# Kernel tuning notes

Measured on AMD Instinct MI355X. Metric: run time of the kernel, lower is better.

Reference implementation:

```python
import math
import jax, jax.numpy as jnp
import numpy as np

B, H, L, Dh = 4, 8, 4096, 64
TOPK_FACTOR = 1.0


def setup_inputs() -> dict:
    key = jax.random.key(0)
    kq, kk, kv = jax.random.split(key, 3)
    shape = (B, H, L, Dh)
    return {
        "q": jax.random.normal(kq, shape, dtype=jnp.float32),
        "k": jax.random.normal(kk, shape, dtype=jnp.float32),
        "v": jax.random.normal(kv, shape, dtype=jnp.float32),
    }


def reference(q, k, v):
    b, h, length, dh = q.shape
    # FFT cross-correlation over the time axis, averaged over Dh -> (B,H,L)
    qf = jnp.fft.rfft(q, axis=2)
    kf = jnp.fft.rfft(k, axis=2)
    corr = jnp.fft.irfft(qf * jnp.conj(kf), n=length, axis=2).mean(axis=-1)
    # top-k delays (k_top is static: depends only on L)
    k_top = max(1, int(TOPK_FACTOR * math.log(length + 1)))
    weights, delays = jax.lax.top_k(corr, k_top)  # (B,H,K)
    attn = jax.nn.softmax(weights, axis=-1)       # (B,H,K)
    # circular-shift gather: idx[b,h,t,j] = (t - delay[b,h,j]) mod L
    t = jnp.arange(length)
    idx = (t[None, None, :, None] - delays[:, :, None, :]) % length  # (B,H,L,K)
    # gathered: (B,H,L,K,Dh)
    gathered = jnp.take_along_axis(v[:, :, :, None, :], idx[..., None], axis=2)
    out = (gathered * attn[:, :, None, :, None]).sum(axis=3)  # (B,H,L,Dh)
    return out
```

## Files before the change

kernel.cpp:

```cpp
#include <hip/hip_runtime.h>
#include <math.h>

#define LEN 4096
#define LOG2LEN 12
#define DH 64
#define NBH 32
#define KTOP 8
#define DPB 4
#define NGRP (DH / DPB)

#define ZT_ELEMS ((size_t)NBH * DH * LEN)
#define TW_N (LEN / 2)
#define SPEC_F2 (NBH * LEN)
#define PART_F2 ((size_t)NBH * NGRP * LEN)

#define XSTR 272

__device__ __forceinline__ int rev16_12(int x) {
  return ((x & 15) << 8) | (x & 240) | (x >> 8);
}

template <int SIM>
__device__ __forceinline__ void twget(const float2* __restrict__ tw, int e,
                                      float& wr, float& wi) {
  const float2 t = tw[e & (TW_N - 1)];
  const float sgn = (e & TW_N) ? -1.0f : 1.0f;
  wr = sgn * t.x;
  wi = sgn * (float)SIM * t.y;
}

struct cf { float r, i; };
__device__ __forceinline__ cf cadd(const cf a, const cf b) { return {a.r + b.r, a.i + b.i}; }
__device__ __forceinline__ cf csub(const cf a, const cf b) { return {a.r - b.r, a.i - b.i}; }
__device__ __forceinline__ cf cmul(const cf a, const float wr, const float wi) {
  return {a.r * wr - a.i * wi, a.r * wi + a.i * wr};
}
template <int S>
__device__ __forceinline__ cf cmuli(const cf a) {
  return (S < 0) ? cf{a.i, -a.r} : cf{-a.i, a.r};
}
template <int S>
__device__ __forceinline__ cf twc(const cf a, const float c, const float s) {
  return cmul(a, c, (S < 0) ? -s : s);
}
template <int S>
__device__ __forceinline__ void r4(cf& a, cf& b, cf& c, cf& d) {
  const cf t0 = cadd(a, c), t1 = csub(a, c), t2 = cadd(b, d), t3 = csub(b, d);
  const cf j3 = cmuli<S>(t3);
  a = cadd(t0, t2); c = csub(t0, t2);
  b = cadd(t1, j3); d = csub(t1, j3);
}
template <int S>
__device__ __forceinline__ void dft16(cf* x) {
  r4<S>(x[0], x[4], x[8], x[12]);
  r4<S>(x[1], x[5], x[9], x[13]);
  r4<S>(x[2], x[6], x[10], x[14]);
  r4<S>(x[3], x[7], x[11], x[15]);
  const float C1 = 0.92387953251128675613f;
  const float S1 = 0.38268343236508977173f;
  const float R2 = 0.70710678118654752440f;
  x[5] = twc<S>(x[5], C1, S1);
  x[6] = twc<S>(x[6], R2, R2);
  x[7] = twc<S>(x[7], S1, C1);
  x[9] = twc<S>(x[9], R2, R2);
  x[10] = cmuli<S>(x[10]);
  x[11] = twc<S>(x[11], -R2, R2);
  x[13] = twc<S>(x[13], S1, C1);
  x[14] = twc<S>(x[14], -R2, R2);
  x[15] = twc<S>(x[15], -C1, -S1);
  r4<S>(x[0], x[1], x[2], x[3]);
  r4<S>(x[4], x[5], x[6], x[7]);
  r4<S>(x[8], x[9], x[10], x[11]);
  r4<S>(x[12], x[13], x[14], x[15]);
  cf t;
  t = x[1]; x[1] = x[4]; x[4] = t;
  t = x[2]; x[2] = x[8]; x[8] = t;
  t = x[3]; x[3] = x[12]; x[12] = t;
  t = x[6]; x[6] = x[9]; x[9] = t;
  t = x[7]; x[7] = x[13]; x[13] = t;
  t = x[11]; x[11] = x[14]; x[14] = t;
}

__global__ void ac_twinit(float2* __restrict__ tw) {
  const int j = blockIdx.x * 256 + threadIdx.x;
  if (j < TW_N) {
    float s, c;
    sincosf(6.2831853071795864769f * (float)j / (float)LEN, &s, &c);
    tw[j] = make_float2(c, s);
  }
}

__global__ __launch_bounds__(256, 4) void ac_transpose(const float* __restrict__ q,
                                                       const float* __restrict__ k,
                                                       float2* __restrict__ zT,
                                                       float2* __restrict__ tw) {
  if (blockIdx.x < 8) {
    const int j = blockIdx.x * 256 + threadIdx.x;
    float s, c;
    sincosf(6.2831853071795864769f * (float)j / (float)LEN, &s, &c);
    tw[j] = make_float2(c, s);
  }
  __shared__ float tq[64][65], tk[64][65];
  const int bh = blockIdx.x >> 6;
  const int t0 = (blockIdx.x & 63) * 64;
  const int tid = threadIdx.x;
  const int tl = tid >> 2;
  const int c = tid & 3;
  const float* qb = q + ((size_t)bh * LEN + t0) * DH;
  const float* kb = k + ((size_t)bh * LEN + t0) * DH;
#pragma unroll
  for (int r = 0; r < 4; ++r) {
    const int d0 = (c + r * 4) * 4;
    const float4 vq = *reinterpret_cast<const float4*>(qb + (size_t)tl * DH + d0);
    const float4 vk = *reinterpret_cast<const float4*>(kb + (size_t)tl * DH + d0);
    tq[tl][d0] = vq.x; tq[tl][d0 + 1] = vq.y; tq[tl][d0 + 2] = vq.z; tq[tl][d0 + 3] = vq.w;
    tk[tl][d0] = vk.x; tk[tl][d0 + 1] = vk.y; tk[tl][d0 + 2] = vk.z; tk[tl][d0 + 3] = vk.w;
  }
  __syncthreads();
  const int d = tid >> 2;
  const int s = tid & 3;
  float2* ob = zT + ((size_t)(bh * DH + d)) * LEN + t0;
#pragma unroll
  for (int r = 0; r < 8; ++r) {
    const int t = (s + r * 4) * 2;
    const float4 o = make_float4(tq[t][d], tk[t][d], tq[t + 1][d], tk[t + 1][d]);
    *reinterpret_cast<float4*>(&ob[t]) = o;
  }
}

template <bool TR>
__global__ __launch_bounds__(256, 2) void ac_fft_fwd(const float* __restrict__ q,
                                                     const float* __restrict__ k,
                                                     const float2* __restrict__ zin,
                                                     const float2* __restrict__ tw,
                                                     float2* __restrict__ part) {
  __shared__ float lre[16 * XSTR], lim[16 * XSTR];
  __shared__ float2 acc[LEN];
  const int tid = threadIdx.x;
  const int hi = tid >> 4, lo = tid & 15;
  const int bh = blockIdx.x / NGRP;
  const int g = blockIdx.x % NGRP;

#pragma unroll
  for (int i = 0; i < 16; ++i) acc[tid + 256 * i] = make_float2(0.f, 0.f);

  for (int dd = 0; dd < DPB; ++dd) {
    const int d = g * DPB + dd;
    cf x[16];
    if (TR) {
      const float2* zb = zin + (size_t)(bh * DH + d) * LEN;
#pragma unroll
      for (int n1 = 0; n1 < 16; ++n1) {
        const float2 z = zb[tid + 256 * n1];
        x[n1].r = z.x; x[n1].i = z.y;
      }
    } else {
      const float* qb = q + (size_t)bh * LEN * DH + d;
      const float* kb = k + (size_t)bh * LEN * DH + d;
#pragma unroll
      for (int n1 = 0; n1 < 16; ++n1) {
        x[n1].r = qb[(size_t)(tid + 256 * n1) * DH];
        x[n1].i = kb[(size_t)(tid + 256 * n1) * DH];
      }
    }
    dft16<-1>(x);
#pragma unroll
    for (int k1 = 1; k1 < 16; ++k1) {
      float wr, wi;
      twget<-1>(tw, tid * k1, wr, wi);
      x[k1] = cmul(x[k1], wr, wi);
    }
    __syncthreads();
#pragma unroll
    for (int k1 = 0; k1 < 16; ++k1) {
      lre[k1 * XSTR + tid] = x[k1].r;
      lim[k1 * XSTR + tid] = x[k1].i;
    }
    __syncthreads();
#pragma unroll
    for (int m1 = 0; m1 < 16; ++m1) {
      const int a = hi * XSTR + 16 * m1 + lo;
      x[m1].r = lre[a]; x[m1].i = lim[a];
    }
    dft16<-1>(x);
#pragma unroll
    for (int j1 = 1; j1 < 16; ++j1) {
      float wr, wi;
      twget<-1>(tw, 16 * lo * j1, wr, wi);
      x[j1] = cmul(x[j1], wr, wi);
    }
    __syncthreads();
#pragma unroll
    for (int j1 = 0; j1 < 16; ++j1) {
      lre[hi * XSTR + 16 * j1 + lo] = x[j1].r;
      lim[hi * XSTR + 16 * j1 + lo] = x[j1].i;
    }
    __syncthreads();
#pragma unroll
    for (int m2 = 0; m2 < 16; ++m2) {
      const int a = hi * XSTR + 16 * lo + m2;
      x[m2].r = lre[a]; x[m2].i = lim[a];
    }
    dft16<-1>(x);
    __syncthreads();
#pragma unroll
    for (int j2 = 0; j2 < 16; ++j2) {
      lre[hi * XSTR + 16 * lo + j2] = x[j2].r;
      lim[hi * XSTR + 16 * lo + j2] = x[j2].i;
    }
    __syncthreads();
#pragma unroll
    for (int i = 0; i < 16; ++i) {
      const int p = tid + 256 * i;
      const int f = rev16_12(p);
      const int f2 = (LEN - f) & (LEN - 1);
      const int p2 = rev16_12(f2);
      const int a1 = i * XSTR + tid;
      const int a2 = (p2 >> 8) * XSTR + (p2 & 255);
      const float ar = lre[a1], ai = lim[a1];
      const float br = lre[a2], bi = lim[a2];
      float2 a = acc[p];
      a.x += 0.5f * (ar * bi + ai * br);
      a.y += 0.25f * ((ar * ar + ai * ai) - (br * br + bi * bi));
      acc[p] = a;
    }
  }
  float2* op = part + (size_t)(bh * NGRP + g) * LEN;
#pragma unroll
  for (int i = 0; i < 16; ++i) {
    const int p = tid + 256 * i;
    op[p] = acc[p];
  }
}

__global__ __launch_bounds__(256) void ac_reduce(const float2* __restrict__ part,
                                                 float2* __restrict__ spec) {
  const int bh = blockIdx.x >> 4;
  const int p = ((blockIdx.x & 15) << 8) | threadIdx.x;
  float accr = 0.f, acci = 0.f;
#pragma unroll 4
  for (int g = 0; g < NGRP; ++g) {
    const float2 v = part[((size_t)(bh * NGRP + g) << LOG2LEN) + p];
    accr += v.x; acci += v.y;
  }
  spec[((size_t)bh << LOG2LEN) + p] = make_float2(accr, acci);
}

__global__ __launch_bounds__(256, 4) void ac_fft_inv(const float2* __restrict__ spec,
                                                     const float2* __restrict__ tw,
                                                     float* __restrict__ attn,
                                                     int* __restrict__ delays) {
  __shared__ float lre[16 * XSTR], lim[16 * XSTR];
  __shared__ float rv[256];
  __shared__ int ri[256];
  __shared__ float selv[KTOP];
  __shared__ int seli[KTOP];
  const int bh = blockIdx.x;
  const int tid = threadIdx.x;
  const int hi = tid >> 4, lo = tid & 15;
  const float2* sp = spec + ((size_t)bh << LOG2LEN);

  cf x[16];
#pragma unroll
  for (int f2 = 0; f2 < 16; ++f2) {
    const float2 z = sp[16 * tid + f2];
    x[f2].r = z.x; x[f2].i = z.y;
  }
  dft16<1>(x);
#pragma unroll
  for (int t0 = 1; t0 < 16; ++t0) {
    float wr, wi;
    twget<1>(tw, 16 * lo * t0, wr, wi);
    x[t0] = cmul(x[t0], wr, wi);
  }
#pragma unroll
  for (int t0 = 0; t0 < 16; ++t0) {
    lre[hi * XSTR + 16 * t0 + lo] = x[t0].r;
    lim[hi * XSTR + 16 * t0 + lo] = x[t0].i;
  }
  __syncthreads();
#pragma unroll
  for (int f1 = 0; f1 < 16; ++f1) {
    const int a = hi * XSTR + 16 * lo + f1;
    x[f1].r = lre[a]; x[f1].i = lim[a];
  }
  dft16<1>(x);
#pragma unroll
  for (int t1 = 0; t1 < 16; ++t1) {
    float wr, wi;
    twget<1>(tw, hi * (16 * t1 + lo), wr, wi);
    x[t1] = cmul(x[t1], wr, wi);
  }
  __syncthreads();
#pragma unroll
  for (int t1 = 0; t1 < 16; ++t1) {
    lre[hi * XSTR + 16 * t1 + lo] = x[t1].r;
    lim[hi * XSTR + 16 * t1 + lo] = x[t1].i;
  }
  __syncthreads();
#pragma unroll
  for (int f0 = 0; f0 < 16; ++f0) {
    const int a = f0 * XSTR + 16 * hi + lo;
    x[f0].r = lre[a]; x[f0].i = lim[a];
  }
  dft16<1>(x);
  __syncthreads();
  const float scale = 1.0f / ((float)LEN * (float)DH);
#pragma unroll
  for (int t2 = 0; t2 < 16; ++t2) lre[256 * t2 + tid] = x[t2].r * scale;
  __syncthreads();

  for (int kk = 0; kk < KTOP; ++kk) {
    float mv = -3.0e38f;
    int mi = 0;
    for (int t = tid; t < LEN; t += 256) {
      const float xv = lre[t];
      if (xv > mv) { mv = xv; mi = t; }
    }
    rv[tid] = mv; ri[tid] = mi;
    __syncthreads();
    for (int s = 128; s > 0; s >>= 1) {
      if (tid < s) {
        if (rv[tid + s] > rv[tid]) { rv[tid] = rv[tid + s]; ri[tid] = ri[tid + s]; }
      }
      __syncthreads();
    }
    if (tid == 0) {
      selv[kk] = rv[0];
      seli[kk] = ri[0];
      lre[ri[0]] = -3.0e38f;
    }
    __syncthreads();
  }
  if (tid == 0) {
    const float mx = selv[0];
    float ex[KTOP];
    float sum = 0.f;
    for (int j = 0; j < KTOP; ++j) { ex[j] = expf(selv[j] - mx); sum += ex[j]; }
    const float inv = 1.0f / sum;
    for (int j = 0; j < KTOP; ++j) {
      attn[bh * KTOP + j] = ex[j] * inv;
      delays[bh * KTOP + j] = seli[j];
    }
  }
}

__global__ __launch_bounds__(256) void ac_gather(const float* __restrict__ v,
                                                 const float* __restrict__ attn,
                                                 const int* __restrict__ delays,
                                                 float* __restrict__ out) {
  const int bx = blockIdx.x;
  const int xcd = bx & 7;
  const int i = bx >> 3;
  const int bh = (xcd << 2) | (i & 3);
  const int chunk = i >> 2;
  const int tid = threadIdx.x;
  float aw[KTOP];
  int dl[KTOP];
#pragma unroll
  for (int j = 0; j < KTOP; ++j) {
    aw[j] = attn[bh * KTOP + j];
    dl[j] = delays[bh * KTOP + j];
  }
  const int e = chunk * 1024 + tid * 4;
  const int t = e >> 6;
  const int d = e & 63;
  const float* vb = v + (size_t)bh * LEN * DH;
  float4 acc = make_float4(0.f, 0.f, 0.f, 0.f);
#pragma unroll
  for (int j = 0; j < KTOP; ++j) {
    int src = t - dl[j];
    if (src < 0) src += LEN;
    const float4 vv = *reinterpret_cast<const float4*>(vb + (size_t)src * DH + d);
    acc.x += aw[j] * vv.x;
    acc.y += aw[j] * vv.y;
    acc.z += aw[j] * vv.z;
    acc.w += aw[j] * vv.w;
  }
  *reinterpret_cast<float4*>(out + (size_t)bh * LEN * DH + e) = acc;
}

extern "C" void kernel_launch(void* const* d_in, const int* in_sizes, int n_in,
                              void* d_out, int out_size, void* d_ws, size_t ws_size,
                              hipStream_t stream) {
  const float* q = (const float*)d_in[0];
  const float* k = (const float*)d_in[1];
  const float* v = (const float*)d_in[2];
  float* out = (float*)d_out;

  const size_t need = (size_t)TW_N * 8 + ZT_ELEMS * 8 + PART_F2 * 8 +
                      (size_t)SPEC_F2 * 8 + (size_t)NBH * KTOP * 8;
  const bool tr = (ws_size >= need);

  float2* tw = (float2*)d_ws;
  float2* zT = tw + TW_N;
  float2* part = tr ? (zT + ZT_ELEMS) : zT;
  float2* spec = part + PART_F2;
  float* attn = (float*)(spec + SPEC_F2);
  int* delays = (int*)(attn + NBH * KTOP);

  if (tr) {
    ac_transpose<<<dim3(NBH * 64), dim3(256), 0, stream>>>(q, k, zT, tw);
    ac_fft_fwd<true><<<dim3(NBH * NGRP), dim3(256), 0, stream>>>(q, k, zT, tw, part);
  } else {
    ac_twinit<<<dim3(8), dim3(256), 0, stream>>>(tw);
    ac_fft_fwd<false><<<dim3(NBH * NGRP), dim3(256), 0, stream>>>(q, k, zT, tw, part);
  }
  ac_reduce<<<dim3(NBH * 16), dim3(256), 0, stream>>>(part, spec);
  ac_fft_inv<<<dim3(NBH), dim3(256), 0, stream>>>(spec, tw, attn, delays);
  ac_gather<<<dim3(NBH * 256), dim3(256), 0, stream>>>(v, attn, delays, out);
}
```

Before: 97.50 us.

## Drop transpose, twiddle table and reduce kernels; compute twiddles by recurrence

Removes the transpose kernel and the twiddle-table setup, so the forward FFT reads q/k directly with strided loads. Twiddles are now computed in registers from one sincos per stage plus complex-multiply recurrence instead of being read from a global table. The separate reduce kernel is folded into the inverse FFT, which sums the 16 partial spectra while loading them. Block ids in the forward FFT are remapped to spread tasks differently across the device. This cuts two launches and the intermediate global traffic, at the cost of uncoalesced strided loads, recurrence rounding error in the twiddles, and a serial 16-way reduction inside only 32 blocks.

```diff
diff --git a/kernel.cpp b/kernel.cpp
--- a/kernel.cpp
+++ b/kernel.cpp
@@ -9,24 +9,13 @@
 #define DPB 4
 #define NGRP (DH / DPB)
 
-#define ZT_ELEMS ((size_t)NBH * DH * LEN)
-#define TW_N (LEN / 2)
-#define SPEC_F2 (NBH * LEN)
 #define PART_F2 ((size_t)NBH * NGRP * LEN)
+#define TWO_PI 6.2831853071795864769f
 
 #define XSTR 272
 
 __device__ __forceinline__ int rev16_12(int x) {
   return ((x & 15) << 8) | (x & 240) | (x >> 8);
-}
-
-template <int SIM>
-__device__ __forceinline__ void twget(const float2* __restrict__ tw, int e,
-                                      float& wr, float& wi) {
-  const float2 t = tw[e & (TW_N - 1)];
-  const float sgn = (e & TW_N) ? -1.0f : 1.0f;
-  wr = sgn * t.x;
-  wi = sgn * (float)SIM * t.y;
 }
 
 struct cf { float r, i; };
@@ -81,94 +70,47 @@
   t = x[11]; x[11] = x[14]; x[14] = t;
 }
 
-__global__ void ac_twinit(float2* __restrict__ tw) {
-  const int j = blockIdx.x * 256 + threadIdx.x;
-  if (j < TW_N) {
-    float s, c;
-    sincosf(6.2831853071795864769f * (float)j / (float)LEN, &s, &c);
-    tw[j] = make_float2(c, s);
-  }
-}
-
-__global__ __launch_bounds__(256, 4) void ac_transpose(const float* __restrict__ q,
-                                                       const float* __restrict__ k,
-                                                       float2* __restrict__ zT,
-                                                       float2* __restrict__ tw) {
-  if (blockIdx.x < 8) {
-    const int j = blockIdx.x * 256 + threadIdx.x;
-    float s, c;
-    sincosf(6.2831853071795864769f * (float)j / (float)LEN, &s, &c);
-    tw[j] = make_float2(c, s);
-  }
-  __shared__ float tq[64][65], tk[64][65];
-  const int bh = blockIdx.x >> 6;
-  const int t0 = (blockIdx.x & 63) * 64;
-  const int tid = threadIdx.x;
-  const int tl = tid >> 2;
-  const int c = tid & 3;
-  const float* qb = q + ((size_t)bh * LEN + t0) * DH;
-  const float* kb = k + ((size_t)bh * LEN + t0) * DH;
-#pragma unroll
-  for (int r = 0; r < 4; ++r) {
-    const int d0 = (c + r * 4) * 4;
-    const float4 vq = *reinterpret_cast<const float4*>(qb + (size_t)tl * DH + d0);
-    const float4 vk = *reinterpret_cast<const float4*>(kb + (size_t)tl * DH + d0);
-    tq[tl][d0] = vq.x; tq[tl][d0 + 1] = vq.y; tq[tl][d0 + 2] = vq.z; tq[tl][d0 + 3] = vq.w;
-    tk[tl][d0] = vk.x; tk[tl][d0 + 1] = vk.y; tk[tl][d0 + 2] = vk.z; tk[tl][d0 + 3] = vk.w;
-  }
-  __syncthreads();
-  const int d = tid >> 2;
-  const int s = tid & 3;
-  float2* ob = zT + ((size_t)(bh * DH + d)) * LEN + t0;
-#pragma unroll
-  for (int r = 0; r < 8; ++r) {
-    const int t = (s + r * 4) * 2;
-    const float4 o = make_float4(tq[t][d], tk[t][d], tq[t + 1][d], tk[t + 1][d]);
-    *reinterpret_cast<float4*>(&ob[t]) = o;
-  }
-}
-
-template <bool TR>
 __global__ __launch_bounds__(256, 2) void ac_fft_fwd(const float* __restrict__ q,
                                                      const float* __restrict__ k,
-                                                     const float2* __restrict__ zin,
-                                                     const float2* __restrict__ tw,
                                                      float2* __restrict__ part) {
   __shared__ float lre[16 * XSTR], lim[16 * XSTR];
   __shared__ float2 acc[LEN];
   const int tid = threadIdx.x;
   const int hi = tid >> 4, lo = tid & 15;
-  const int bh = blockIdx.x / NGRP;
-  const int g = blockIdx.x % NGRP;
+  const int bid = (int)blockIdx.x;
+  const int task = ((bid & 7) << 6) | (bid >> 3);
+  const int bh = task >> 4;
+  const int g = task & 15;
+
+  float s1, c1, s2, c2;
+  sincosf(-TWO_PI * (float)tid / (float)LEN, &s1, &c1);
+  sincosf(-TWO_PI * (float)lo / 256.0f, &s2, &c2);
 
 #pragma unroll
   for (int i = 0; i < 16; ++i) acc[tid + 256 * i] = make_float2(0.f, 0.f);
 
+  const float* qb = q + (size_t)bh * LEN * DH + 4 * g;
+  const float* kb = k + (size_t)bh * LEN * DH + 4 * g;
+
+#pragma unroll 1
   for (int dd = 0; dd < DPB; ++dd) {
-    const int d = g * DPB + dd;
     cf x[16];
-    if (TR) {
-      const float2* zb = zin + (size_t)(bh * DH + d) * LEN;
-#pragma unroll
-      for (int n1 = 0; n1 < 16; ++n1) {
-        const float2 z = zb[tid + 256 * n1];
-        x[n1].r = z.x; x[n1].i = z.y;
+#pragma unroll
+    for (int n1 = 0; n1 < 16; ++n1) {
+      const size_t off = (size_t)(tid + 256 * n1) * DH + dd;
+      x[n1].r = qb[off];
+      x[n1].i = kb[off];
+    }
+    dft16<-1>(x);
+    {
+      float cr = c1, ci = s1;
+#pragma unroll
+      for (int k1 = 1; k1 < 16; ++k1) {
+        x[k1] = cmul(x[k1], cr, ci);
+        const float nr = cr * c1 - ci * s1;
+        ci = cr * s1 + ci * c1;
+        cr = nr;
       }
-    } else {
-      const float* qb = q + (size_t)bh * LEN * DH + d;
-      const float* kb = k + (size_t)bh * LEN * DH + d;
-#pragma unroll
-      for (int n1 = 0; n1 < 16; ++n1) {
-        x[n1].r = qb[(size_t)(tid + 256 * n1) * DH];
-        x[n1].i = kb[(size_t)(tid + 256 * n1) * DH];
-      }
-    }
-    dft16<-1>(x);
-#pragma unroll
-    for (int k1 = 1; k1 < 16; ++k1) {
-      float wr, wi;
-      twget<-1>(tw, tid * k1, wr, wi);
-      x[k1] = cmul(x[k1], wr, wi);
     }
     __syncthreads();
 #pragma unroll
@@ -183,11 +125,15 @@
       x[m1].r = lre[a]; x[m1].i = lim[a];
     }
     dft16<-1>(x);
-#pragma unroll
-    for (int j1 = 1; j1 < 16; ++j1) {
-      float wr, wi;
-      twget<-1>(tw, 16 * lo * j1, wr, wi);
-      x[j1] = cmul(x[j1], wr, wi);
+    {
+      float cr = c2, ci = s2;
+#pragma unroll
+      for (int j1 = 1; j1 < 16; ++j1) {
+        x[j1] = cmul(x[j1], cr, ci);
+        const float nr = cr * c2 - ci * s2;
+        ci = cr * s2 + ci * c2;
+        cr = nr;
+      }
     }
     __syncthreads();
 #pragma unroll
@@ -233,21 +179,7 @@
   }
 }
 
-__global__ __launch_bounds__(256) void ac_reduce(const float2* __restrict__ part,
-                                                 float2* __restrict__ spec) {
-  const int bh = blockIdx.x >> 4;
-  const int p = ((blockIdx.x & 15) << 8) | threadIdx.x;
-  float accr = 0.f, acci = 0.f;
-#pragma unroll 4
-  for (int g = 0; g < NGRP; ++g) {
-    const float2 v = part[((size_t)(bh * NGRP + g) << LOG2LEN) + p];
-    accr += v.x; acci += v.y;
-  }
-  spec[((size_t)bh << LOG2LEN) + p] = make_float2(accr, acci);
-}
-
-__global__ __launch_bounds__(256, 4) void ac_fft_inv(const float2* __restrict__ spec,
-                                                     const float2* __restrict__ tw,
+__global__ __launch_bounds__(256, 2) void ac_fft_inv(const float2* __restrict__ part,
                                                      float* __restrict__ attn,
                                                      int* __restrict__ delays) {
   __shared__ float lre[16 * XSTR], lim[16 * XSTR];
@@ -258,20 +190,36 @@
   const int bh = blockIdx.x;
   const int tid = threadIdx.x;
   const int hi = tid >> 4, lo = tid & 15;
-  const float2* sp = spec + ((size_t)bh << LOG2LEN);
 
   cf x[16];
 #pragma unroll
-  for (int f2 = 0; f2 < 16; ++f2) {
-    const float2 z = sp[16 * tid + f2];
-    x[f2].r = z.x; x[f2].i = z.y;
-  }
+  for (int f2 = 0; f2 < 16; ++f2) { x[f2].r = 0.f; x[f2].i = 0.f; }
+  const float2* pb = part + ((size_t)bh * NGRP) * LEN + 16 * tid;
+  for (int g = 0; g < NGRP; ++g) {
+    const float4* b4 = reinterpret_cast<const float4*>(pb + (size_t)g * LEN);
+#pragma unroll
+    for (int i = 0; i < 8; ++i) {
+      const float4 vv = b4[i];
+      x[2 * i].r += vv.x; x[2 * i].i += vv.y;
+      x[2 * i + 1].r += vv.z; x[2 * i + 1].i += vv.w;
+    }
+  }
+
+  float sA, cA, sB0, cB0, sBs, cBs;
+  sincosf(TWO_PI * (float)lo / 256.0f, &sA, &cA);
+  sincosf(TWO_PI * (float)(hi * lo) / (float)LEN, &sB0, &cB0);
+  sincosf(TWO_PI * (float)hi / 256.0f, &sBs, &cBs);
+
   dft16<1>(x);
-#pragma unroll
-  for (int t0 = 1; t0 < 16; ++t0) {
-    float wr, wi;
-    twget<1>(tw, 16 * lo * t0, wr, wi);
-    x[t0] = cmul(x[t0], wr, wi);
+  {
+    float cr = cA, ci = sA;
+#pragma unroll
+    for (int t0 = 1; t0 < 16; ++t0) {
+      x[t0] = cmul(x[t0], cr, ci);
+      const float nr = cr * cA - ci * sA;
+      ci = cr * sA + ci * cA;
+      cr = nr;
+    }
   }
 #pragma unroll
   for (int t0 = 0; t0 < 16; ++t0) {
@@ -285,11 +233,15 @@
     x[f1].r = lre[a]; x[f1].i = lim[a];
   }
   dft16<1>(x);
-#pragma unroll
-  for (int t1 = 0; t1 < 16; ++t1) {
-    float wr, wi;
-    twget<1>(tw, hi * (16 * t1 + lo), wr, wi);
-    x[t1] = cmul(x[t1], wr, wi);
+  {
+    float cr = cB0, ci = sB0;
+#pragma unroll
+    for (int t1 = 0; t1 < 16; ++t1) {
+      x[t1] = cmul(x[t1], cr, ci);
+      const float nr = cr * cBs - ci * sBs;
+      ci = cr * sBs + ci * cBs;
+      cr = nr;
+    }
   }
   __syncthreads();
 #pragma unroll
@@ -388,25 +340,11 @@
   const float* v = (const float*)d_in[2];
   float* out = (float*)d_out;
 
-  const size_t need = (size_t)TW_N * 8 + ZT_ELEMS * 8 + PART_F2 * 8 +
-                      (size_t)SPEC_F2 * 8 + (size_t)NBH * KTOP * 8;
-  const bool tr = (ws_size >= need);
-
-  float2* tw = (float2*)d_ws;
-  float2* zT = tw + TW_N;
-  float2* part = tr ? (zT + ZT_ELEMS) : zT;
-  float2* spec = part + PART_F2;
-  float* attn = (float*)(spec + SPEC_F2);
+  float2* part = (float2*)d_ws;
+  float* attn = (float*)(part + PART_F2);
   int* delays = (int*)(attn + NBH * KTOP);
 
-  if (tr) {
-    ac_transpose<<<dim3(NBH * 64), dim3(256), 0, stream>>>(q, k, zT, tw);
-    ac_fft_fwd<true><<<dim3(NBH * NGRP), dim3(256), 0, stream>>>(q, k, zT, tw, part);
-  } else {
-    ac_twinit<<<dim3(8), dim3(256), 0, stream>>>(tw);
-    ac_fft_fwd<false><<<dim3(NBH * NGRP), dim3(256), 0, stream>>>(q, k, zT, tw, part);
-  }
-  ac_reduce<<<dim3(NBH * 16), dim3(256), 0, stream>>>(part, spec);
-  ac_fft_inv<<<dim3(NBH), dim3(256), 0, stream>>>(spec, tw, attn, delays);
+  ac_fft_fwd<<<dim3(NBH * NGRP), dim3(256), 0, stream>>>(q, k, part);
+  ac_fft_inv<<<dim3(NBH), dim3(256), 0, stream>>>(part, attn, delays);
   ac_gather<<<dim3(NBH * 256), dim3(256), 0, stream>>>(v, attn, delays, out);
 }
```

Measured after the change: 170.4 us. 74.8% more time.
